# Optimization experiments

Hardware: AMD Instinct MI355X
Metric: run time of the kernel (lower is better)

The kernel has to match this reference:

```python
import jax, jax.numpy as jnp
import numpy as np

IN_FEATURES = 8192
OUT_FEATURES = 28672
BATCH = 8  # tokens; skinny GEMM -> memory-bound weight streaming


def setup_inputs() -> dict:
    key = jax.random.key(0)
    k1, k2, k3, k4 = jax.random.split(key, 4)
    x = jax.random.normal(k1, (BATCH, IN_FEATURES), dtype=jnp.float32)
    # ternary codes in {0,1,2} -> weight values {-1,0,+1}; pack 4 codes / byte
    codes = jax.random.randint(k2, (OUT_FEATURES, IN_FEATURES), 0, 3, dtype=jnp.int32)
    codes4 = codes.reshape(OUT_FEATURES, IN_FEATURES // 4, 4)
    shifts = jnp.array([0, 2, 4, 6], dtype=jnp.int32)
    packed_weight = jnp.sum(codes4 << shifts, axis=-1).astype(jnp.int32)  # [O, I//4]
    weight_scale = jax.random.uniform(k3, (1,), dtype=jnp.float32, minval=0.01, maxval=0.1)
    bias = jax.random.normal(k4, (OUT_FEATURES,), dtype=jnp.float32)
    return {"x": x, "packed_weight": packed_weight, "weight_scale": weight_scale, "bias": bias}


def _unpack_ternary(packed):
    # [O, I//4] int -> [O, I] ternary in {-1,0,1}
    shifts = jnp.array([0, 2, 4, 6], dtype=jnp.int32)
    w = ((packed[:, :, None] >> shifts) & 3) - 1  # [O, I//4, 4]
    return w.reshape(packed.shape[0], -1)


def reference(x, packed_weight, weight_scale, bias):
    B = x.shape[0]
    x_flat = x.reshape(B, IN_FEATURES)
    # per-tensor absmax int8 activation quantization
    absmax = jnp.maximum(jnp.max(jnp.abs(x_flat)), 1e-5)
    act_scale = absmax / 127.0
    x_q = jnp.clip(jnp.round(x_flat / act_scale), -128, 127)  # int8 values, kept f32
    w = _unpack_ternary(packed_weight).astype(jnp.float32)  # [O, I]
    # fused dequant GEMM: integer-valued accumulation, single scalar scale
    acc = jnp.einsum('bi,oi->bo', x_q, w)  # exact in f32 (|acc| << 2^24)
    scale = weight_scale[0] * act_scale
    out = acc * scale + bias
    return out.reshape(B, OUT_FEATURES)
```

## Files before the change

### kernel.cpp

```cpp
#include <hip/hip_runtime.h>
#include <stdint.h>

#define O_FEATS 28672
#define I_FEATS 8192
#define BATCH 8
#define PITCH_W 260

typedef int i32x4 __attribute__((ext_vector_type(4)));


static __device__ __forceinline__ int unpack4(uint32_t p) {
  uint32_t lo = p & 0x0Fu;
  uint32_t hi = (p >> 4) & 0x0Fu;
  uint32_t a = (lo * 0x41u) & 0x0303u;
  uint32_t b = (hi * 0x41u) & 0x0303u;
  return (int)(a | (b << 16));
}

__global__ void k_absmax(const float* __restrict__ x, uint32_t* __restrict__ ws) {
  __shared__ float red[4];
  int t = threadIdx.x;
  float4 v = ((const float4*)x)[blockIdx.x * 256 + t];
  float m = fmaxf(fmaxf(fabsf(v.x), fabsf(v.y)), fmaxf(fabsf(v.z), fabsf(v.w)));
#pragma unroll
  for (int off = 32; off; off >>= 1)
    m = fmaxf(m, __shfl_xor(m, off));
  if ((t & 63) == 0) red[t >> 6] = m;
  __syncthreads();
  if (t == 0)
    ws[16 + blockIdx.x] =
        __float_as_uint(fmaxf(fmaxf(red[0], red[1]), fmaxf(red[2], red[3])));
}

__global__ void k_quant(const float* __restrict__ x, uint32_t* __restrict__ ws) {
  __shared__ float s_amax;
  __shared__ int reds[4];
  int t = threadIdx.x;
  if (blockIdx.x >= 64) {
    int row = 8 + ((blockIdx.x - 64) >> 3), seg = blockIdx.x & 7;
    int k0 = seg * 1024 + t * 4;
    int S = k0 >> 6, g = (k0 >> 4) & 3, j = k0 & 15;
    ws[1024 + ((S * 1024 + (g * 16 + row) * 16 + j) >> 2)] = 0u;
    return;
  }
  int b = blockIdx.x >> 3, seg = blockIdx.x & 7;
  if (t < 64) {
    float m = __uint_as_float(ws[16 + t]);
#pragma unroll
    for (int off = 32; off; off >>= 1)
      m = fmaxf(m, __shfl_xor(m, off));
    if (t == 0) {
      float a = fmaxf(m, 1e-5f);
      s_amax = a;
      ws[0] = __float_as_uint(a);
    }
  }
  __syncthreads();
  float s = s_amax / 127.0f;
  float4 v = ((const float4*)(x + b * I_FEATS + seg * 1024))[t];
  int q0 = (int)fminf(fmaxf(rintf(v.x / s), -128.f), 127.f);
  int q1 = (int)fminf(fmaxf(rintf(v.y / s), -128.f), 127.f);
  int q2 = (int)fminf(fmaxf(rintf(v.z / s), -128.f), 127.f);
  int q3 = (int)fminf(fmaxf(rintf(v.w / s), -128.f), 127.f);
  uint32_t pk = (uint32_t)(q0 & 0xff) | ((uint32_t)(q1 & 0xff) << 8) |
                ((uint32_t)(q2 & 0xff) << 16) | ((uint32_t)(q3 & 0xff) << 24);
  {
    int k0 = seg * 1024 + t * 4;
    int S = k0 >> 6, g = (k0 >> 4) & 3, j = k0 & 15;
    ws[1024 + ((S * 1024 + (g * 16 + b) * 16 + j) >> 2)] = pk;
  }
  int s4 = q0 + q1 + q2 + q3;
#pragma unroll
  for (int off = 32; off; off >>= 1)
    s4 += __shfl_xor(s4, off);
  if ((t & 63) == 0) reds[t >> 6] = s4;
  __syncthreads();
  if (t == 0)
    ws[128 + blockIdx.x] = (uint32_t)(reds[0] + reds[1] + reds[2] + reds[3]);
}

__global__ void __launch_bounds__(256, 4)
k_gemm(const int* __restrict__ Wp, const float* __restrict__ wscale,
       const float* __restrict__ bias, const uint32_t* __restrict__ ws,
       float* __restrict__ out) {
  __shared__ uint32_t Wlds[16 * PITCH_W];
  __shared__ int red[4][32][4];
  __shared__ int s_sumx[BATCH];
  __shared__ float s_scale;

  const int t = threadIdx.x;
  const int wave = t >> 6, lane = t & 63;

  if (t < 64) {
    int p = (int)ws[128 + t];
    p += __shfl_xor(p, 1);
    p += __shfl_xor(p, 2);
    p += __shfl_xor(p, 4);
    if ((t & 7) == 0) s_sumx[t >> 3] = p;
    if (t == 0) s_scale = (__uint_as_float(ws[0]) / 127.0f) * wscale[0];
  }

  const int o_base = blockIdx.x * 16;
  const int m = lane & 15, g = lane >> 4;

  const uint8_t* xqT = (const uint8_t*)(ws + 1024);
  const int4* ap = (const int4*)(xqT + (size_t)(wave * 4) * 1024 + lane * 16);

  const uint8_t* src_base =
      (const uint8_t*)Wp + (size_t)(o_base + wave * 4) * 8192 + lane * 16;
  uint32_t* lds_row0 = &Wlds[(wave * 4) * PITCH_W];

  const uint32_t* bp0 = &Wlds[m * PITCH_W + (wave * 256 + g * 16) / 4];

  i32x4 acc = {0, 0, 0, 0};

  for (int c = 0; c < 8; ++c) {
    __syncthreads();
#pragma unroll
    for (int i = 0; i < 4; ++i) {
      const uint32_t* src = (const uint32_t*)(src_base + (size_t)i * 8192 + c * 1024);
      __builtin_amdgcn_global_load_lds(src, lds_row0 + i * PITCH_W, 16, 0, 0);
    }
    int4 a[4];
#pragma unroll
    for (int s = 0; s < 4; ++s) a[s] = ap[(c * 16 + s) * 64];
    __syncthreads();
#pragma unroll
    for (int s = 0; s < 4; ++s) {
      int4 b = *(const int4*)(bp0 + s * 16);
      i32x4 af, bf;
      af.x = a[s].x; af.y = a[s].y; af.z = a[s].z; af.w = a[s].w;
      bf.x = unpack4((uint32_t)b.x);
      bf.y = unpack4((uint32_t)b.y);
      bf.z = unpack4((uint32_t)b.z);
      bf.w = unpack4((uint32_t)b.w);
      acc = __builtin_amdgcn_mfma_i32_16x16x64_i8(af, bf, acc, 0, 0, 0);
    }
  }

  if (lane < 32) {
#pragma unroll
    for (int r = 0; r < 4; ++r) red[wave][lane][r] = acc[r];
  }
  __syncthreads();

  if (t < 32) {
    const int n = t & 15;
    const int q = t >> 4;
    const int o = o_base + n;
    const float bo = bias[o];
#pragma unroll
    for (int r = 0; r < 4; ++r) {
      int mm = q * 4 + r;
      int tot = red[0][t][r] + red[1][t][r] + red[2][t][r] + red[3][t][r];
      out[mm * O_FEATS + o] = (float)(tot - s_sumx[mm]) * s_scale + bo;
    }
  }
}

extern "C" void kernel_launch(void* const* d_in, const int* in_sizes, int n_in,
                              void* d_out, int out_size, void* d_ws, size_t ws_size,
                              hipStream_t stream) {
  const float* x = (const float*)d_in[0];
  const int* pw = (const int*)d_in[1];
  const float* wscale = (const float*)d_in[2];
  const float* bias = (const float*)d_in[3];
  float* out = (float*)d_out;
  uint32_t* ws = (uint32_t*)d_ws;

  k_absmax<<<64, 256, 0, stream>>>(x, ws);
  k_quant<<<128, 256, 0, stream>>>(x, ws);
  k_gemm<<<O_FEATS / 16, 256, 0, stream>>>(pw, wscale, bias, ws, out);
}
```

Measured before the change: 320.9 us.

## Double-buffer weight chunks in LDS with vmcnt-based barriers and chunk permutation

The GEMM's weight staging becomes double-buffered in LDS: the next 1KB-per-row chunk and its activations are prefetched while the current chunk is unpacked and fed to MFMA. Manual s_waitcnt vmcnt/lgkmcnt barriers replace the two __syncthreads per iteration. The chunk order is also permuted per block (XOR with blockIdx&7) to spread memory accesses. This doubles the LDS footprint (about 33KB), which may reduce occupancy below the launch-bounds target, and the hand-tuned vmcnt count must match the number of outstanding loads.

```diff
diff --git a/kernel.cpp b/kernel.cpp
--- a/kernel.cpp
+++ b/kernel.cpp
@@ -4,9 +4,14 @@
 #define O_FEATS 28672
 #define I_FEATS 8192
 #define BATCH 8
-#define PITCH_W 260
+#define PITCH_CB 1040
+#define CHUNK_B (16 * PITCH_CB)
 
 typedef int i32x4 __attribute__((ext_vector_type(4)));
+
+#define BAR_VM8  asm volatile("s_waitcnt vmcnt(8)\n\ts_barrier" ::: "memory")
+#define BAR_VM0  asm volatile("s_waitcnt vmcnt(0)\n\ts_barrier" ::: "memory")
+#define BAR_LGKM asm volatile("s_waitcnt lgkmcnt(0)\n\ts_barrier" ::: "memory")
 
 
 static __device__ __forceinline__ int unpack4(uint32_t p) {
@@ -83,7 +88,7 @@
 k_gemm(const int* __restrict__ Wp, const float* __restrict__ wscale,
        const float* __restrict__ bias, const uint32_t* __restrict__ ws,
        float* __restrict__ out) {
-  __shared__ uint32_t Wlds[16 * PITCH_W];
+  __shared__ uint8_t Wlds[2 * CHUNK_B];
   __shared__ int red[4][32][4];
   __shared__ int s_sumx[BATCH];
   __shared__ float s_scale;
@@ -99,43 +104,65 @@
     if ((t & 7) == 0) s_sumx[t >> 3] = p;
     if (t == 0) s_scale = (__uint_as_float(ws[0]) / 127.0f) * wscale[0];
   }
+  __syncthreads();
 
   const int o_base = blockIdx.x * 16;
   const int m = lane & 15, g = lane >> 4;
-
+  const int perm = blockIdx.x & 7;
+
+  const uint8_t* W8 = (const uint8_t*)Wp;
   const uint8_t* xqT = (const uint8_t*)(ws + 1024);
-  const int4* ap = (const int4*)(xqT + (size_t)(wave * 4) * 1024 + lane * 16);
-
-  const uint8_t* src_base =
-      (const uint8_t*)Wp + (size_t)(o_base + wave * 4) * 8192 + lane * 16;
-  uint32_t* lds_row0 = &Wlds[(wave * 4) * PITCH_W];
-
-  const uint32_t* bp0 = &Wlds[m * PITCH_W + (wave * 256 + g * 16) / 4];
+
+  const uint8_t* gsrc = W8 + (size_t)(o_base + wave * 4) * 8192 + lane * 16;
+  uint8_t* ldst = Wlds + (wave * 4) * PITCH_CB;
+  const uint8_t* fbase = Wlds + m * PITCH_CB + wave * 256 + g * 16;
+
+#define STAGE_W(buf, cc)                                                      \
+  {                                                                           \
+    const uint8_t* gs = gsrc + (cc) * 1024;                                   \
+    uint8_t* ld = ldst + (buf) * CHUNK_B;                                     \
+    _Pragma("unroll") for (int i = 0; i < 4; ++i)                             \
+        __builtin_amdgcn_global_load_lds((const uint32_t*)(gs + i * 8192),    \
+                                         (uint32_t*)(ld + i * PITCH_CB), 16,  \
+                                         0, 0);                               \
+  }
+#define LOAD_A(dst, cc)                                                       \
+  {                                                                           \
+    _Pragma("unroll") for (int s = 0; s < 4; ++s)(dst)[s] =                   \
+        *(const int4*)(xqT + (size_t)(((cc) * 16 + wave * 4 + s) << 10) +     \
+                       lane * 16);                                            \
+  }
 
   i32x4 acc = {0, 0, 0, 0};
-
+  int4 acur[4], anext[4];
+
+  STAGE_W(0, (0 ^ perm));
+  LOAD_A(acur, (0 ^ perm));
+
+#pragma unroll
   for (int c = 0; c < 8; ++c) {
-    __syncthreads();
-#pragma unroll
-    for (int i = 0; i < 4; ++i) {
-      const uint32_t* src = (const uint32_t*)(src_base + (size_t)i * 8192 + c * 1024);
-      __builtin_amdgcn_global_load_lds(src, lds_row0 + i * PITCH_W, 16, 0, 0);
-    }
-    int4 a[4];
-#pragma unroll
-    for (int s = 0; s < 4; ++s) a[s] = ap[(c * 16 + s) * 64];
-    __syncthreads();
+    if (c < 7) {
+      STAGE_W((c + 1) & 1, ((c + 1) ^ perm));
+      LOAD_A(anext, ((c + 1) ^ perm));
+      BAR_VM8;
+    } else {
+      BAR_VM0;
+    }
+    const uint8_t* fb = fbase + (c & 1) * CHUNK_B;
 #pragma unroll
     for (int s = 0; s < 4; ++s) {
-      int4 b = *(const int4*)(bp0 + s * 16);
-      i32x4 af, bf;
-      af.x = a[s].x; af.y = a[s].y; af.z = a[s].z; af.w = a[s].w;
-      bf.x = unpack4((uint32_t)b.x);
-      bf.y = unpack4((uint32_t)b.y);
-      bf.z = unpack4((uint32_t)b.z);
-      bf.w = unpack4((uint32_t)b.w);
+      int4 bw = *(const int4*)(fb + s * 64);
+      i32x4 bf, af;
+      bf.x = unpack4((uint32_t)bw.x);
+      bf.y = unpack4((uint32_t)bw.y);
+      bf.z = unpack4((uint32_t)bw.z);
+      bf.w = unpack4((uint32_t)bw.w);
+      af.x = acur[s].x; af.y = acur[s].y; af.z = acur[s].z; af.w = acur[s].w;
       acc = __builtin_amdgcn_mfma_i32_16x16x64_i8(af, bf, acc, 0, 0, 0);
     }
+    BAR_LGKM;
+#pragma unroll
+    for (int s = 0; s < 4; ++s) acur[s] = anext[s];
   }
 
   if (lane < 32) {
@@ -143,10 +170,8 @@
     for (int r = 0; r < 4; ++r) red[wave][lane][r] = acc[r];
   }
   __syncthreads();
-
   if (t < 32) {
-    const int n = t & 15;
-    const int q = t >> 4;
+    const int n = t & 15, q = t >> 4;
     const int o = o_base + n;
     const float bo = bias[o];
 #pragma unroll
@@ -156,6 +181,8 @@
       out[mm * O_FEATS + o] = (float)(tot - s_sumx[mm]) * s_scale + bo;
     }
   }
+#undef STAGE_W
+#undef LOAD_A
 }
 
 extern "C" void kernel_launch(void* const* d_in, const int* in_sizes, int n_in,
```

Result: slower. 338.0 us (+5.3%).
